# Optimization experiments

Measured on AMD Instinct MI355X. Metric: run time of the kernel, lower is better.

Reference implementation:

```python
import jax, jax.numpy as jnp
import numpy as np

N_NODES = 100000
N_EDGES = 1600000
N_GRAPHS = 1000
NODES_PER_GRAPH = 100  # batch vector is arange(N)//100: exactly 100 nodes per graph
HID = 32
MAX_Z = 1000
K = 30
D_LAT = HID * 3 + 1  # 97, total_latent_dim


def setup_inputs() -> dict:
    key = jax.random.key(0)
    ks = jax.random.split(key, 24)
    s = 1.0 / np.sqrt(HID)
    inp = {
        "z": jax.random.randint(ks[0], (N_NODES,), 0, MAX_Z, dtype=jnp.int32),
        "edge_index": jax.random.randint(ks[1], (2, N_EDGES), 0, N_NODES, dtype=jnp.int32),
        "batch": (jnp.arange(N_NODES, dtype=jnp.int32) // NODES_PER_GRAPH),
        "edge_weight": jax.random.uniform(ks[2], (N_EDGES,), jnp.float32, 0.1, 1.0),
        "z_emb": jax.random.normal(ks[3], (MAX_Z, HID), jnp.float32) * 0.1,
        # GCNConv stack: [32->32, 32->32, 32->32, 32->1]
        "Wg1": jax.random.normal(ks[4], (HID, HID)) * s,
        "bg1": jnp.zeros((HID,), jnp.float32),
        "Wg2": jax.random.normal(ks[5], (HID, HID)) * s,
        "bg2": jnp.zeros((HID,), jnp.float32),
        "Wg3": jax.random.normal(ks[6], (HID, HID)) * s,
        "bg3": jnp.zeros((HID,), jnp.float32),
        "Wg4": jax.random.normal(ks[7], (HID, 1)) * s,
        "bg4": jnp.zeros((1,), jnp.float32),
        # Conv1d(1, 16, kernel=97, stride=97)
        "Wc1": jax.random.normal(ks[8], (16, D_LAT)) * (1.0 / np.sqrt(D_LAT)),
        "bc1": jnp.zeros((16,), jnp.float32),
        # Conv1d(16, 32, kernel=5, stride=1)
        "Wc2": jax.random.normal(ks[9], (32, 16, 5)) * (1.0 / np.sqrt(16 * 5)),
        "bc2": jnp.zeros((32,), jnp.float32),
        # Linear(352, 128), Linear(128, 1)
        "Wl1": jax.random.normal(ks[10], (352, 128)) * (1.0 / np.sqrt(352)),
        "bl1": jnp.zeros((128,), jnp.float32),
        "Wl2": jax.random.normal(ks[11], (128, 1)) * (1.0 / np.sqrt(128)),
        "bl2": jnp.zeros((1,), jnp.float32),
    }
    return inp


def gcn_conv(x, src, dst, ew, W, b, n):
    # PyG GCNConv: xW, add self-loops (weight 1), sym-normalize, aggregate at dst, + bias
    xw = x @ W
    deg = jax.ops.segment_sum(ew, dst, num_segments=n) + 1.0  # +1 for self loop
    dinv = jnp.where(deg > 0, jax.lax.rsqrt(deg), 0.0)
    norm = dinv[src] * ew * dinv[dst]                          # [E]
    out = jax.ops.segment_sum(norm[:, None] * xw[src], dst, num_segments=n)
    out = out + xw * (dinv * dinv)[:, None]                    # self-loop term
    return out + b


def _forward(z, edge_index, batch, edge_weight, z_emb, Wg1, bg1, Wg2, bg2, Wg3, bg3,
             Wg4, bg4, Wc1, bc1, Wc2, bc2, Wl1, bl1, Wl2, bl2):
    src, dst = edge_index[0], edge_index[1]
    n = z.shape[0]
    x = z_emb[z]                                              # [N, 32]
    xs = []
    h = x
    for W, b in ((Wg1, bg1), (Wg2, bg2), (Wg3, bg3), (Wg4, bg4)):
        h = jnp.tanh(gcn_conv(h, src, dst, edge_weight, W, b, n))
        xs.append(h)
    x = jnp.concatenate(xs, axis=-1)                          # [N, 97]
    # global_sort_pool: batch is uniform (100 nodes/graph) so dense batching is a reshape
    dense = x.reshape(N_GRAPHS, NODES_PER_GRAPH, D_LAT)       # [B, 100, 97]
    idx = jnp.argsort(-dense[:, :, -1], axis=1)[:, :K]        # sort desc by last channel
    top = jnp.take_along_axis(dense, idx[:, :, None], axis=1)  # [B, 30, 97]
    # Conv1d(1,16,97,stride=97) on flattened [B,1,30*97] == per-slot dense layer
    y = jax.nn.relu(jnp.einsum('bkd,cd->bck', top, Wc1) + bc1[None, :, None])  # [B,16,30]
    y = y.reshape(N_GRAPHS, 16, K // 2, 2).max(axis=-1)        # MaxPool1d(2,2) -> [B,16,15]
    y = jax.lax.conv_general_dilated(y, Wc2, (1,), 'VALID',
                                     dimension_numbers=('NCH', 'OIH', 'NCH'))
    y = jax.nn.relu(y + bc2[None, :, None])                    # [B,32,11]
    y = y.reshape(N_GRAPHS, -1)                                # [B,352]
    y = jax.nn.relu(y @ Wl1 + bl1)                             # dropout: eval mode, identity
    return y @ Wl2 + bl2                                       # [B,1]


def reference(z, edge_index, batch, edge_weight, z_emb, Wg1, bg1, Wg2, bg2, Wg3, bg3,
              Wg4, bg4, Wc1, bc1, Wc2, bc2, Wl1, bl1, Wl2, bl2):
    return _forward(z, edge_index, batch, edge_weight, z_emb, Wg1, bg1, Wg2, bg2, Wg3,
                    bg3, Wg4, bg4, Wc1, bc1, Wc2, bc2, Wl1, bl1, Wl2, bl2)
```

## Files before the change

### kernel.cpp

```cpp
#include <hip/hip_runtime.h>

#define HID 32
#define DLAT 97
#define NPG 100
#define TOPK 30
#define BKT_NODES 128
#define BKT_SHIFT 7
#define NBUCK 1024
#define CAPF 2432
#define CHUNK 8192

__global__ __launch_bounds__(256) void binB1_kernel(
    const int* __restrict__ src, const int* __restrict__ dst,
    const float* __restrict__ ew, int* __restrict__ gcursor,
    int2* __restrict__ bedge, int E) {
    __shared__ int hist[NBUCK];
    __shared__ int lcur[NBUCK];
    __shared__ int dcache[CHUNK];
    for (int i = threadIdx.x; i < NBUCK; i += 256) hist[i] = 0;
    __syncthreads();
    int base = blockIdx.x * CHUNK;
    int M = min(E - base, CHUNK);
    for (int i = threadIdx.x; i < M; i += 256) {
        int d = dst[base + i];
        dcache[i] = d;
        atomicAdd(&hist[d >> BKT_SHIFT], 1);
    }
    __syncthreads();
    for (int b = threadIdx.x; b < NBUCK; b += 256) {
        int v = hist[b];
        lcur[b] = b * CAPF + (v ? atomicAdd(&gcursor[b], v) : 0);
    }
    __syncthreads();
    for (int i = threadIdx.x; i < M; i += 256) {
        int d = dcache[i];
        int slot = atomicAdd(&lcur[d >> BKT_SHIFT], 1);
        bedge[slot] = make_int2(src[base + i] | ((d & (BKT_NODES - 1)) << 20),
                                __float_as_int(ew[base + i]));
    }
}

__global__ __launch_bounds__(256) void sortlocal2_kernel(
    const int2* __restrict__ bedge, const int* __restrict__ gcursor,
    const int* __restrict__ z, const float* __restrict__ z_emb,
    const float* __restrict__ W1, int2* __restrict__ csr,
    int* __restrict__ row_start, int* __restrict__ row_deg,
    float* __restrict__ dinv, float* __restrict__ xw_a, int N) {
    __shared__ int2 LDSe[CAPF];
    __shared__ int sh256[256];
    __shared__ int cnt[BKT_NODES];
    __shared__ int sh2[BKT_NODES];
    __shared__ int lc2[BKT_NODES];
    __shared__ int zloc[BKT_NODES];
    __shared__ float dloc[BKT_NODES];
    __shared__ float W1L[HID * HID];
    __shared__ int bstart_s;

    int b = blockIdx.x, t = threadIdx.x;

    int t4 = t * 4;
    int a0 = gcursor[t4], a1 = gcursor[t4 + 1], a2 = gcursor[t4 + 2], a3 = gcursor[t4 + 3];
    int tsum = a0 + a1 + a2 + a3;
    sh256[t] = tsum;
    for (int i = t; i < HID * HID; i += 256) W1L[i] = W1[i];
    if (t < BKT_NODES) cnt[t] = 0;
    __syncthreads();
    for (int off = 1; off < 256; off <<= 1) {
        int tv = (t >= off) ? sh256[t - off] : 0;
        __syncthreads();
        sh256[t] += tv;
        __syncthreads();
    }
    if (t == (b >> 2)) {
        int e = sh256[t] - tsum;
        int bb = b & 3;
        if (bb > 0) e += a0;
        if (bb > 1) e += a1;
        if (bb > 2) e += a2;
        bstart_s = e;
    }
    __syncthreads();
    const int begOut = bstart_s;
    const int M = gcursor[b];

    for (int i = t; i < M; i += 256) {
        int2 e = bedge[(size_t)b * CAPF + i];
        LDSe[i] = e;
        atomicAdd(&cnt[(e.x >> 20) & (BKT_NODES - 1)], 1);
    }
    __syncthreads();
    int v = 0, excl = 0;
    int n = b * BKT_NODES + t;
    if (t < BKT_NODES) { v = cnt[t]; sh2[t] = v; }
    __syncthreads();
    for (int off = 1; off < BKT_NODES; off <<= 1) {
        int tv = (t >= off && t < BKT_NODES) ? sh2[t - off] : 0;
        __syncthreads();
        if (t < BKT_NODES) sh2[t] += tv;
        __syncthreads();
    }
    if (t < BKT_NODES) {
        excl = sh2[t] - v;
        lc2[t] = excl;
        if (n < N) {
            row_start[n] = begOut + excl;
            row_deg[n] = v;
        }
    }
    __syncthreads();
    for (int i = t; i < M; i += 256) {
        int2 e = LDSe[i];
        int slot = atomicAdd(&lc2[(e.x >> 20) & (BKT_NODES - 1)], 1);
        csr[begOut + slot] = make_int2(e.x & 0xFFFFF, e.y);
    }
    __syncthreads();
    if (t < BKT_NODES && n < N) {
        float s = 1.f;
        int s0 = begOut + excl;
        for (int i = 0; i < v; ++i) s += __int_as_float(csr[s0 + i].y);
        float di = 1.f / sqrtf(s);
        dinv[n] = di;
        dloc[t] = di;
        zloc[t] = z[n];
    }
    __syncthreads();
    int lim = min(BKT_NODES, N - b * BKT_NODES);
    if (lim > 0) {
        for (int idx = t; idx < lim * HID; idx += 256) {
            int nl = idx >> 5, f = idx & 31;
            const float* row = z_emb + (size_t)zloc[nl] * HID;
            float s = 0.f;
#pragma unroll
            for (int k = 0; k < HID; ++k) s += row[k] * W1L[k * HID + f];
            xw_a[(size_t)(b * BKT_NODES + nl) * HID + f] = s * dloc[nl];
        }
    }
}

template <int MODE>
__global__ __launch_bounds__(256) void agg32v_kernel(
    const int* __restrict__ row_start, const int* __restrict__ row_deg,
    const int2* __restrict__ csr, const float* __restrict__ xw,
    const float* __restrict__ b, const float* __restrict__ dinv,
    const float* __restrict__ Wn, float* __restrict__ cout,
    float* __restrict__ xw4, int N) {
    int tid = blockIdx.x * blockDim.x + threadIdx.x;
    int n = tid >> 5;
    if (n >= N) return;
    int lane = threadIdx.x & 31;
    int eq = lane & 3;
    int f4 = lane & 28;
    int beg = row_start[n];
    int end = beg + row_deg[n];
    float4 acc = make_float4(0.f, 0.f, 0.f, 0.f);
    for (int i = beg; i < end; i += 16) {
        int2 cw[4];
        float w[4];
#pragma unroll
        for (int j = 0; j < 4; ++j) {
            int e = i + 4 * j + eq;
            cw[j] = csr[min(e, end - 1)];
            w[j] = (e < end) ? __int_as_float(cw[j].y) : 0.f;
        }
        float4 x[4];
#pragma unroll
        for (int j = 0; j < 4; ++j)
            x[j] = *(const float4*)(xw + (size_t)cw[j].x * HID + f4);
#pragma unroll
        for (int j = 0; j < 4; ++j) {
            acc.x += w[j] * x[j].x;
            acc.y += w[j] * x[j].y;
            acc.z += w[j] * x[j].z;
            acc.w += w[j] * x[j].w;
        }
    }
#pragma unroll
    for (int m = 1; m <= 2; m <<= 1) {
        acc.x += __shfl_xor(acc.x, m, 32);
        acc.y += __shfl_xor(acc.y, m, 32);
        acc.z += __shfl_xor(acc.z, m, 32);
        acc.w += __shfl_xor(acc.w, m, 32);
    }
    float s = (eq == 0) ? acc.x : (eq == 1) ? acc.y : (eq == 2) ? acc.z : acc.w;
    float di = dinv[n];
    float outv = tanhf(di * (s + xw[(size_t)n * HID + lane]) + b[lane]);
    cout[(size_t)n * HID + lane] = outv;

    if (MODE == 1) {
        float p = outv * Wn[lane];
        p += __shfl_xor(p, 16, 32);
        p += __shfl_xor(p, 8, 32);
        p += __shfl_xor(p, 4, 32);
        p += __shfl_xor(p, 2, 32);
        p += __shfl_xor(p, 1, 32);
        if (lane == 0) xw4[n] = p * di;
    }
}

__global__ __launch_bounds__(256) void xwgemm_kernel(
    const float* __restrict__ h, const float* __restrict__ Wn,
    const float* __restrict__ dinv, float* __restrict__ xw_next, int N) {
    __shared__ float4 WnL[HID * 8];
    int tid = threadIdx.x;
    WnL[tid] = ((const float4*)Wn)[tid];
    __syncthreads();
    int n = blockIdx.x * 256 + tid;
    if (n >= N) return;
    const float4* hr = (const float4*)(h + (size_t)n * HID);
    float4 acc[8];
#pragma unroll
    for (int fb = 0; fb < 8; ++fb) acc[fb] = make_float4(0.f, 0.f, 0.f, 0.f);
#pragma unroll
    for (int k4 = 0; k4 < 8; ++k4) {
        float4 h4 = hr[k4];
#pragma unroll
        for (int kk = 0; kk < 4; ++kk) {
            float hk = (kk == 0) ? h4.x : (kk == 1) ? h4.y : (kk == 2) ? h4.z : h4.w;
            int k = k4 * 4 + kk;
#pragma unroll
            for (int fb = 0; fb < 8; ++fb) {
                float4 w4 = WnL[k * 8 + fb];
                acc[fb].x += hk * w4.x;
                acc[fb].y += hk * w4.y;
                acc[fb].z += hk * w4.z;
                acc[fb].w += hk * w4.w;
            }
        }
    }
    float di = dinv[n];
    float4* o = (float4*)(xw_next + (size_t)n * HID);
#pragma unroll
    for (int fb = 0; fb < 8; ++fb) {
        acc[fb].x *= di; acc[fb].y *= di; acc[fb].z *= di; acc[fb].w *= di;
        o[fb] = acc[fb];
    }
}

__global__ __launch_bounds__(256) void topk_head_kernel(
    const int* __restrict__ row_start, const int* __restrict__ row_deg,
    const int2* __restrict__ csr, const float* __restrict__ xw4,
    const float* __restrict__ b4, const float* __restrict__ dinv,
    const float* __restrict__ cblk,
    const float* __restrict__ Wc1, const float* __restrict__ bc1,
    const float* __restrict__ Wc2, const float* __restrict__ bc2,
    const float* __restrict__ Wl1, const float* __restrict__ bl1,
    const float* __restrict__ Wl2, const float* __restrict__ bl2,
    float* __restrict__ out, int N) {
    int g = blockIdx.x;
    int tid = threadIdx.x;
    __shared__ float v[NPG];
    __shared__ int tidx[TOPK];
    __shared__ float tval[TOPK];
    __shared__ float top[TOPK * DLAT];
    __shared__ float Wc1L[16 * DLAT];
    __shared__ float Wc2L[32 * 16 * 5];
    __shared__ float y1[16 * TOPK];
    __shared__ float y2[16 * 15];
    __shared__ float y3[352];
    __shared__ float r[256];

    for (int i = tid; i < 16 * DLAT; i += 256) Wc1L[i] = Wc1[i];
    for (int i = tid; i < 32 * 16 * 5; i += 256) Wc2L[i] = Wc2[i];

    if (tid < NPG) {
        int n = g * NPG + tid;
        int beg = row_start[n], end = beg + row_deg[n];
        float s0 = 0.f, s1 = 0.f;
        for (int i = beg; i < end; i += 4) {
            int2 e0 = csr[min(i, end - 1)];
            int2 e1 = csr[min(i + 1, end - 1)];
            int2 e2 = csr[min(i + 2, end - 1)];
            int2 e3 = csr[min(i + 3, end - 1)];
            float x0 = xw4[e0.x], x1 = xw4[e1.x], x2 = xw4[e2.x], x3 = xw4[e3.x];
            s0 += __int_as_float(e0.y) * x0;
            if (i + 1 < end) s1 += __int_as_float(e1.y) * x1;
            if (i + 2 < end) s0 += __int_as_float(e2.y) * x2;
            if (i + 3 < end) s1 += __int_as_float(e3.y) * x3;
        }
        v[tid] = tanhf(dinv[n] * ((s0 + s1) + xw4[n]) + b4[0]);
    }
    __syncthreads();
    if (tid < NPG) {
        float vi = v[tid];
        int cnt = 0;
#pragma unroll 4
        for (int j = 0; j < NPG; ++j) {
            float vj = v[j];
            cnt += (vj > vi) || (vj == vi && j < tid);
        }
        if (cnt < TOPK) {
            tidx[cnt] = g * NPG + tid;
            tval[cnt] = vi;
        }
    }
    __syncthreads();

    for (int idx = tid; idx < TOPK * DLAT; idx += 256) {
        int k = idx / DLAT, d = idx - k * DLAT;
        float val;
        if (d == 96) val = tval[k];
        else val = cblk[(size_t)(d >> 5) * N * HID + (size_t)tidx[k] * HID + (d & 31)];
        top[idx] = val;
    }
    __syncthreads();

    for (int idx = tid; idx < 16 * TOPK; idx += 256) {
        int c = idx / TOPK, k = idx % TOPK;
        float s = bc1[c];
        const float* w = Wc1L + c * DLAT;
        const float* t = top + k * DLAT;
#pragma unroll 4
        for (int d = 0; d < DLAT; ++d) s += t[d] * w[d];
        y1[c * TOPK + k] = fmaxf(s, 0.f);
    }
    __syncthreads();

    for (int idx = tid; idx < 16 * 15; idx += 256) {
        int c = idx / 15, j = idx % 15;
        y2[idx] = fmaxf(y1[c * TOPK + 2 * j], y1[c * TOPK + 2 * j + 1]);
    }
    __syncthreads();

    for (int idx = tid; idx < 352; idx += 256) {
        int o = idx / 11, t = idx % 11;
        float s = bc2[o];
#pragma unroll
        for (int i = 0; i < 16; ++i) {
#pragma unroll
            for (int k = 0; k < 5; ++k)
                s += Wc2L[(o * 16 + i) * 5 + k] * y2[i * 15 + t + k];
        }
        y3[idx] = fmaxf(s, 0.f);
    }
    __syncthreads();

    {
        int half = tid >> 7;
        int o = tid & 127;
        int d0 = half * 176;
        float s = (half == 0) ? bl1[o] : 0.f;
#pragma unroll 1
        for (int d = d0; d < d0 + 176; d += 8) {
            float wv[8], yv[8];
#pragma unroll
            for (int j = 0; j < 8; ++j) wv[j] = Wl1[(d + j) * 128 + o];
#pragma unroll
            for (int j = 0; j < 8; ++j) yv[j] = y3[d + j];
#pragma unroll
            for (int j = 0; j < 8; ++j) s += yv[j] * wv[j];
        }
        r[tid] = s;
    }
    __syncthreads();
    if (tid < 128) r[tid] = fmaxf(r[tid] + r[tid + 128], 0.f) * Wl2[tid];
    __syncthreads();
    if (tid < 64) r[tid] += r[tid + 64];
    __syncthreads();
    if (tid == 0) {
        float s = 0.f;
        for (int j = 0; j < 64; ++j) s += r[j];
        out[g] = s + bl2[0];
    }
}


extern "C" void kernel_launch(void* const* d_in, const int* in_sizes, int n_in,
                              void* d_out, int out_size, void* d_ws, size_t ws_size,
                              hipStream_t stream) {
    const int* z = (const int*)d_in[0];
    const int* ei = (const int*)d_in[1];
    const float* ew = (const float*)d_in[3];
    const float* z_emb = (const float*)d_in[4];
    const float* Wg[4] = {(const float*)d_in[5], (const float*)d_in[7],
                          (const float*)d_in[9], (const float*)d_in[11]};
    const float* bg[4] = {(const float*)d_in[6], (const float*)d_in[8],
                          (const float*)d_in[10], (const float*)d_in[12]};
    const float* Wc1 = (const float*)d_in[13];
    const float* bc1 = (const float*)d_in[14];
    const float* Wc2 = (const float*)d_in[15];
    const float* bc2 = (const float*)d_in[16];
    const float* Wl1 = (const float*)d_in[17];
    const float* bl1 = (const float*)d_in[18];
    const float* Wl2 = (const float*)d_in[19];
    const float* bl2 = (const float*)d_in[20];
    float* out = (float*)d_out;

    const int N = in_sizes[0];
    const int E = in_sizes[1] / 2;
    const int G = out_size;
    const int* src = ei;
    const int* dst = ei + E;

    auto cdiv = [](long long a, long long b) { return (int)((a + b - 1) / b); };
    const int NB = cdiv(E, CHUNK);
    const int NBKT = cdiv(N, BKT_NODES);

    char* ws = (char*)d_ws;
    int2* bedge = (int2*)ws;                  ws += sizeof(int2) * (size_t)NBUCK * CAPF;
    int2* csr = (int2*)ws;                    ws += sizeof(int2) * (size_t)E;
    int* gcursor = (int*)ws;                  ws += sizeof(int) * NBUCK;
    int* row_start = (int*)ws;                ws += sizeof(int) * N;
    int* row_deg = (int*)ws;                  ws += sizeof(int) * N;
    float* dinv = (float*)ws;                 ws += sizeof(float) * N;
    float* xw_a = (float*)ws;                 ws += sizeof(float) * (size_t)N * HID;
    float* cblk = (float*)ws;                 ws += sizeof(float) * (size_t)3 * N * HID;
    float* xw4 = (float*)ws;                  ws += sizeof(float) * N;
    float* xw_b = (float*)bedge;
    float* cb0 = cblk;
    float* cb1 = cblk + (size_t)N * HID;
    float* cb2 = cblk + (size_t)2 * N * HID;

    const int B = 256;

    hipMemsetAsync(gcursor, 0, sizeof(int) * NBUCK, stream);
    binB1_kernel<<<NB, B, 0, stream>>>(src, dst, ew, gcursor, bedge, E);
    sortlocal2_kernel<<<NBKT, B, 0, stream>>>(bedge, gcursor, z, z_emb, Wg[0], csr,
                                              row_start, row_deg, dinv, xw_a, N);

    const int AGGB = cdiv((long long)N * 32, B);
    const int GEMB = cdiv(N, B);
    agg32v_kernel<0><<<AGGB, B, 0, stream>>>(row_start, row_deg, csr, xw_a, bg[0], dinv,
                                             Wg[1], cb0, nullptr, N);
    xwgemm_kernel<<<GEMB, B, 0, stream>>>(cb0, Wg[1], dinv, xw_b, N);
    agg32v_kernel<0><<<AGGB, B, 0, stream>>>(row_start, row_deg, csr, xw_b, bg[1], dinv,
                                             Wg[2], cb1, nullptr, N);
    xwgemm_kernel<<<GEMB, B, 0, stream>>>(cb1, Wg[2], dinv, xw_a, N);
    agg32v_kernel<1><<<AGGB, B, 0, stream>>>(row_start, row_deg, csr, xw_a, bg[2], dinv,
                                             Wg[3], cb2, xw4, N);

    topk_head_kernel<<<G, 256, 0, stream>>>(row_start, row_deg, csr, xw4, bg[3], dinv,
                                            cblk, Wc1, bc1, Wc2, bc2, Wl1, bl1,
                                            Wl2, bl2, out, N);
}
```

Baseline: 382.1 us.

## Fuse next-layer XW GEMM into aggregation and hoist bucket scan out of sort

Moves the 32x32 next-layer weight product into the aggregation kernel's epilogue using warp shuffles and an LDS copy of the weights, which removes the two standalone xwgemm launches and the extra read of the hidden activations. The bucket prefix scan now runs once in its own single-block kernel instead of being redone in every sort block. Degree sums are accumulated with float LDS atomics during binning rather than by re-reading CSR rows. The aggregation loop also unrolls to 8 edge groups per iteration for more memory-level parallelism, at the cost of higher register pressure and a per-block LDS weight load.

```diff
diff --git a/kernel.cpp b/kernel.cpp
--- a/kernel.cpp
+++ b/kernel.cpp
@@ -40,53 +40,58 @@
     }
 }
 
-__global__ __launch_bounds__(256) void sortlocal2_kernel(
+__global__ __launch_bounds__(256) void scan1024_kernel(
+    const int* __restrict__ g, int* __restrict__ bstart) {
+    __shared__ int sh[256];
+    int t = threadIdx.x;
+    int t4 = t * 4;
+    int a0 = g[t4], a1 = g[t4 + 1], a2 = g[t4 + 2], a3 = g[t4 + 3];
+    int tsum = a0 + a1 + a2 + a3;
+    sh[t] = tsum;
+    __syncthreads();
+    for (int off = 1; off < 256; off <<= 1) {
+        int tv = (t >= off) ? sh[t - off] : 0;
+        __syncthreads();
+        sh[t] += tv;
+        __syncthreads();
+    }
+    int e = sh[t] - tsum;
+    bstart[t4] = e;
+    bstart[t4 + 1] = e + a0;
+    bstart[t4 + 2] = e + a0 + a1;
+    bstart[t4 + 3] = e + a0 + a1 + a2;
+}
+
+__global__ __launch_bounds__(256) void sortlocal3_kernel(
     const int2* __restrict__ bedge, const int* __restrict__ gcursor,
+    const int* __restrict__ bstart,
     const int* __restrict__ z, const float* __restrict__ z_emb,
     const float* __restrict__ W1, int2* __restrict__ csr,
     int* __restrict__ row_start, int* __restrict__ row_deg,
     float* __restrict__ dinv, float* __restrict__ xw_a, int N) {
     __shared__ int2 LDSe[CAPF];
-    __shared__ int sh256[256];
     __shared__ int cnt[BKT_NODES];
     __shared__ int sh2[BKT_NODES];
     __shared__ int lc2[BKT_NODES];
     __shared__ int zloc[BKT_NODES];
+    __shared__ float wsum[BKT_NODES];
     __shared__ float dloc[BKT_NODES];
     __shared__ float W1L[HID * HID];
-    __shared__ int bstart_s;
 
     int b = blockIdx.x, t = threadIdx.x;
-
-    int t4 = t * 4;
-    int a0 = gcursor[t4], a1 = gcursor[t4 + 1], a2 = gcursor[t4 + 2], a3 = gcursor[t4 + 3];
-    int tsum = a0 + a1 + a2 + a3;
-    sh256[t] = tsum;
     for (int i = t; i < HID * HID; i += 256) W1L[i] = W1[i];
-    if (t < BKT_NODES) cnt[t] = 0;
-    __syncthreads();
-    for (int off = 1; off < 256; off <<= 1) {
-        int tv = (t >= off) ? sh256[t - off] : 0;
-        __syncthreads();
-        sh256[t] += tv;
-        __syncthreads();
-    }
-    if (t == (b >> 2)) {
-        int e = sh256[t] - tsum;
-        int bb = b & 3;
-        if (bb > 0) e += a0;
-        if (bb > 1) e += a1;
-        if (bb > 2) e += a2;
-        bstart_s = e;
-    }
-    __syncthreads();
-    const int begOut = bstart_s;
+    if (t < BKT_NODES) { cnt[t] = 0; wsum[t] = 0.f; }
+    __syncthreads();
+
+    const int begOut = bstart[b];
     const int M = gcursor[b];
 
     for (int i = t; i < M; i += 256) {
         int2 e = bedge[(size_t)b * CAPF + i];
         LDSe[i] = e;
-        atomicAdd(&cnt[(e.x >> 20) & (BKT_NODES - 1)], 1);
+        int nl = (e.x >> 20) & (BKT_NODES - 1);
+        atomicAdd(&cnt[nl], 1);
+        atomicAdd(&wsum[nl], __int_as_float(e.y));
     }
     __syncthreads();
     int v = 0, excl = 0;
@@ -102,9 +107,15 @@
     if (t < BKT_NODES) {
         excl = sh2[t] - v;
         lc2[t] = excl;
+        float di = 1.f / sqrtf(1.f + wsum[t]);
+        dloc[t] = di;
         if (n < N) {
             row_start[n] = begOut + excl;
             row_deg[n] = v;
+            dinv[n] = di;
+            zloc[t] = z[n];
+        } else {
+            zloc[t] = 0;
         }
     }
     __syncthreads();
@@ -113,17 +124,6 @@
         int slot = atomicAdd(&lc2[(e.x >> 20) & (BKT_NODES - 1)], 1);
         csr[begOut + slot] = make_int2(e.x & 0xFFFFF, e.y);
     }
-    __syncthreads();
-    if (t < BKT_NODES && n < N) {
-        float s = 1.f;
-        int s0 = begOut + excl;
-        for (int i = 0; i < v; ++i) s += __int_as_float(csr[s0 + i].y);
-        float di = 1.f / sqrtf(s);
-        dinv[n] = di;
-        dloc[t] = di;
-        zloc[t] = z[n];
-    }
-    __syncthreads();
     int lim = min(BKT_NODES, N - b * BKT_NODES);
     if (lim > 0) {
         for (int idx = t; idx < lim * HID; idx += 256) {
@@ -138,36 +138,44 @@
 }
 
 template <int MODE>
-__global__ __launch_bounds__(256) void agg32v_kernel(
+__global__ __launch_bounds__(256) void agg32w_kernel(
     const int* __restrict__ row_start, const int* __restrict__ row_deg,
     const int2* __restrict__ csr, const float* __restrict__ xw,
     const float* __restrict__ b, const float* __restrict__ dinv,
     const float* __restrict__ Wn, float* __restrict__ cout,
-    float* __restrict__ xw4, int N) {
-    int tid = blockIdx.x * blockDim.x + threadIdx.x;
+    float* __restrict__ xw_next, int N) {
+    __shared__ float WnL[HID * HID];
+    int t = threadIdx.x;
+    if (MODE == 0) {
+        for (int i = t; i < HID * HID; i += 256) WnL[i] = Wn[i];
+    } else {
+        if (t < HID) WnL[t] = Wn[t];
+    }
+    __syncthreads();
+    int tid = blockIdx.x * 256 + t;
     int n = tid >> 5;
     if (n >= N) return;
-    int lane = threadIdx.x & 31;
+    int lane = t & 31;
     int eq = lane & 3;
     int f4 = lane & 28;
     int beg = row_start[n];
     int end = beg + row_deg[n];
     float4 acc = make_float4(0.f, 0.f, 0.f, 0.f);
-    for (int i = beg; i < end; i += 16) {
-        int2 cw[4];
-        float w[4];
-#pragma unroll
-        for (int j = 0; j < 4; ++j) {
+    for (int i = beg; i < end; i += 32) {
+        int2 cw[8];
+        float w[8];
+#pragma unroll
+        for (int j = 0; j < 8; ++j) {
             int e = i + 4 * j + eq;
             cw[j] = csr[min(e, end - 1)];
             w[j] = (e < end) ? __int_as_float(cw[j].y) : 0.f;
         }
-        float4 x[4];
-#pragma unroll
-        for (int j = 0; j < 4; ++j)
+        float4 x[8];
+#pragma unroll
+        for (int j = 0; j < 8; ++j)
             x[j] = *(const float4*)(xw + (size_t)cw[j].x * HID + f4);
 #pragma unroll
-        for (int j = 0; j < 4; ++j) {
+        for (int j = 0; j < 8; ++j) {
             acc.x += w[j] * x[j].x;
             acc.y += w[j] * x[j].y;
             acc.z += w[j] * x[j].z;
@@ -186,53 +194,22 @@
     float outv = tanhf(di * (s + xw[(size_t)n * HID + lane]) + b[lane]);
     cout[(size_t)n * HID + lane] = outv;
 
-    if (MODE == 1) {
-        float p = outv * Wn[lane];
+    if (MODE == 0) {
+        float p = 0.f;
+#pragma unroll
+        for (int k = 0; k < HID; ++k) {
+            float ok = __shfl(outv, k, 32);
+            p += ok * WnL[k * HID + lane];
+        }
+        xw_next[(size_t)n * HID + lane] = p * di;
+    } else {
+        float p = outv * WnL[lane];
         p += __shfl_xor(p, 16, 32);
         p += __shfl_xor(p, 8, 32);
         p += __shfl_xor(p, 4, 32);
         p += __shfl_xor(p, 2, 32);
         p += __shfl_xor(p, 1, 32);
-        if (lane == 0) xw4[n] = p * di;
-    }
-}
-
-__global__ __launch_bounds__(256) void xwgemm_kernel(
-    const float* __restrict__ h, const float* __restrict__ Wn,
-    const float* __restrict__ dinv, float* __restrict__ xw_next, int N) {
-    __shared__ float4 WnL[HID * 8];
-    int tid = threadIdx.x;
-    WnL[tid] = ((const float4*)Wn)[tid];
-    __syncthreads();
-    int n = blockIdx.x * 256 + tid;
-    if (n >= N) return;
-    const float4* hr = (const float4*)(h + (size_t)n * HID);
-    float4 acc[8];
-#pragma unroll
-    for (int fb = 0; fb < 8; ++fb) acc[fb] = make_float4(0.f, 0.f, 0.f, 0.f);
-#pragma unroll
-    for (int k4 = 0; k4 < 8; ++k4) {
-        float4 h4 = hr[k4];
-#pragma unroll
-        for (int kk = 0; kk < 4; ++kk) {
-            float hk = (kk == 0) ? h4.x : (kk == 1) ? h4.y : (kk == 2) ? h4.z : h4.w;
-            int k = k4 * 4 + kk;
-#pragma unroll
-            for (int fb = 0; fb < 8; ++fb) {
-                float4 w4 = WnL[k * 8 + fb];
-                acc[fb].x += hk * w4.x;
-                acc[fb].y += hk * w4.y;
-                acc[fb].z += hk * w4.z;
-                acc[fb].w += hk * w4.w;
-            }
-        }
-    }
-    float di = dinv[n];
-    float4* o = (float4*)(xw_next + (size_t)n * HID);
-#pragma unroll
-    for (int fb = 0; fb < 8; ++fb) {
-        acc[fb].x *= di; acc[fb].y *= di; acc[fb].z *= di; acc[fb].w *= di;
-        o[fb] = acc[fb];
+        if (lane == 0) xw_next[n] = p * di;
     }
 }
 
@@ -399,6 +376,7 @@
     int2* bedge = (int2*)ws;                  ws += sizeof(int2) * (size_t)NBUCK * CAPF;
     int2* csr = (int2*)ws;                    ws += sizeof(int2) * (size_t)E;
     int* gcursor = (int*)ws;                  ws += sizeof(int) * NBUCK;
+    int* bstart = (int*)ws;                   ws += sizeof(int) * NBUCK;
     int* row_start = (int*)ws;                ws += sizeof(int) * N;
     int* row_deg = (int*)ws;                  ws += sizeof(int) * N;
     float* dinv = (float*)ws;                 ws += sizeof(float) * N;
@@ -414,18 +392,16 @@
 
     hipMemsetAsync(gcursor, 0, sizeof(int) * NBUCK, stream);
     binB1_kernel<<<NB, B, 0, stream>>>(src, dst, ew, gcursor, bedge, E);
-    sortlocal2_kernel<<<NBKT, B, 0, stream>>>(bedge, gcursor, z, z_emb, Wg[0], csr,
-                                              row_start, row_deg, dinv, xw_a, N);
+    scan1024_kernel<<<1, B, 0, stream>>>(gcursor, bstart);
+    sortlocal3_kernel<<<NBKT, B, 0, stream>>>(bedge, gcursor, bstart, z, z_emb, Wg[0],
+                                              csr, row_start, row_deg, dinv, xw_a, N);
 
     const int AGGB = cdiv((long long)N * 32, B);
-    const int GEMB = cdiv(N, B);
-    agg32v_kernel<0><<<AGGB, B, 0, stream>>>(row_start, row_deg, csr, xw_a, bg[0], dinv,
-                                             Wg[1], cb0, nullptr, N);
-    xwgemm_kernel<<<GEMB, B, 0, stream>>>(cb0, Wg[1], dinv, xw_b, N);
-    agg32v_kernel<0><<<AGGB, B, 0, stream>>>(row_start, row_deg, csr, xw_b, bg[1], dinv,
-                                             Wg[2], cb1, nullptr, N);
-    xwgemm_kernel<<<GEMB, B, 0, stream>>>(cb1, Wg[2], dinv, xw_a, N);
-    agg32v_kernel<1><<<AGGB, B, 0, stream>>>(row_start, row_deg, csr, xw_a, bg[2], dinv,
+    agg32w_kernel<0><<<AGGB, B, 0, stream>>>(row_start, row_deg, csr, xw_a, bg[0], dinv,
+                                             Wg[1], cb0, xw_b, N);
+    agg32w_kernel<0><<<AGGB, B, 0, stream>>>(row_start, row_deg, csr, xw_b, bg[1], dinv,
+                                             Wg[2], cb1, xw_a, N);
+    agg32w_kernel<1><<<AGGB, B, 0, stream>>>(row_start, row_deg, csr, xw_a, bg[2], dinv,
                                              Wg[3], cb2, xw4, N);
 
     topk_head_kernel<<<G, 256, 0, stream>>>(row_start, row_deg, csr, xw4, bg[3], dinv,
```

Result: faster. 371.5 us (-2.8%).
